# Performance work log

Measured on AMD Instinct MI355X. Metric: run time of the kernel, lower is better.

Reference implementation:

```python
import jax, jax.numpy as jnp
import numpy as np

N_EMBD = 1024
N_HEAD = 16

def _lin_params(key, fan_in, fan_out):
    kw, kb = jax.random.split(key)
    bound = 1.0 / np.sqrt(fan_in)
    W = jax.random.uniform(kw, (fan_in, fan_out), minval=-bound, maxval=bound, dtype=jnp.float32)
    b = jax.random.uniform(kb, (fan_out,), minval=-bound, maxval=bound, dtype=jnp.float32)
    return W, b

def setup_inputs() -> dict:
    key = jax.random.key(0)
    ks = jax.random.split(key, 6)
    x = jax.random.normal(ks[0], (2, 2048, N_EMBD), dtype=jnp.float32)
    W_attn, b_attn = _lin_params(ks[1], N_EMBD, 3 * N_EMBD)
    W_proj, b_proj = _lin_params(ks[2], N_EMBD, N_EMBD)
    W_fc, b_fc = _lin_params(ks[3], N_EMBD, 4 * N_EMBD)
    W_fc2, b_fc2 = _lin_params(ks[4], 4 * N_EMBD, N_EMBD)
    ln1_g = jnp.ones((N_EMBD,), jnp.float32); ln1_b = jnp.zeros((N_EMBD,), jnp.float32)
    ln2_g = jnp.ones((N_EMBD,), jnp.float32); ln2_b = jnp.zeros((N_EMBD,), jnp.float32)
    return {"x": x, "W_attn": W_attn, "b_attn": b_attn, "W_proj": W_proj, "b_proj": b_proj,
            "W_fc": W_fc, "b_fc": b_fc, "W_fc2": W_fc2, "b_fc2": b_fc2,
            "ln1_g": ln1_g, "ln1_b": ln1_b, "ln2_g": ln2_g, "ln2_b": ln2_b}

def _layernorm(x, g, b, eps=1e-5):
    mu = jnp.mean(x, axis=-1, keepdims=True)
    var = jnp.var(x, axis=-1, keepdims=True)
    return (x - mu) * jax.lax.rsqrt(var + eps) * g + b

def _attention(x, W_attn, b_attn, W_proj, b_proj):
    B, T, C = x.shape
    hd = C // N_HEAD
    qkv = x @ W_attn + b_attn                      # [B,T,3C]
    q, k, v = jnp.split(qkv, 3, axis=-1)
    # [B,T,C] -> [B,H,T,hd]
    q = q.reshape(B, T, N_HEAD, hd).transpose(0, 2, 1, 3)
    k = k.reshape(B, T, N_HEAD, hd).transpose(0, 2, 1, 3)
    v = v.reshape(B, T, N_HEAD, hd).transpose(0, 2, 1, 3)
    att = jnp.einsum('bhqd,bhkd->bhqk', q, k) * (1.0 / np.sqrt(hd))
    causal = jnp.tril(jnp.ones((T, T), bool))
    att = jnp.where(causal[None, None], att, -jnp.inf)
    att = jax.nn.softmax(att, axis=-1)
    y = jnp.einsum('bhqk,bhkd->bhqd', att, v)      # [B,H,T,hd]
    y = y.transpose(0, 2, 1, 3).reshape(B, T, C)
    return y @ W_proj + b_proj

def _mlp(x, W_fc, b_fc, W_fc2, b_fc2):
    h = jax.nn.gelu(x @ W_fc + b_fc, approximate=False)
    return h @ W_fc2 + b_fc2

def reference(x, W_attn, b_attn, W_proj, b_proj, W_fc, b_fc, W_fc2, b_fc2,
              ln1_g, ln1_b, ln2_g, ln2_b):
    x = x + _attention(_layernorm(x, ln1_g, ln1_b), W_attn, b_attn, W_proj, b_proj)
    x = x + _mlp(_layernorm(x, ln2_g, ln2_b), W_fc, b_fc, W_fc2, b_fc2)
    return x
```

## Files before the change

kernel.cpp:

```cpp
#include <hip/hip_runtime.h>
#include <cstdint>
#include <cstddef>


typedef unsigned short u16;
typedef short bf16x8 __attribute__((ext_vector_type(8)));
typedef float f32x4 __attribute__((ext_vector_type(4)));

#define C_EMBD 1024
#define T_SEQ  2048
#define N_BATCH 2
#define N_HEADS 16
#define HEAD_D 64
#define M_TOK  4096
#define Q_SCALE 0.18033688011112042f

__device__ __forceinline__ u16 f2b(float f) {
  union { float f; unsigned u; } v; v.f = f;
  unsigned r = (v.u + 0x7fffu + ((v.u >> 16) & 1u)) >> 16;
  return (u16)r;
}
__device__ __forceinline__ float b2f(u16 u) {
  union { unsigned u; float f; } v; v.u = ((unsigned)u) << 16;
  return v.f;
}
__device__ __forceinline__ unsigned pk2(float a, float b) {
  union { float f; unsigned u; } x, y; x.f = a; y.f = b;
  return __builtin_amdgcn_perm(y.u, x.u, 0x07060302u);
}
__device__ __forceinline__ void load_lds16(const void* g, void* l) {
  __builtin_amdgcn_global_load_lds(
      (const __attribute__((address_space(1))) void*)g,
      (__attribute__((address_space(3))) void*)l, 16, 0, 0);
}
__device__ __forceinline__ float gelu_fast(float x) {
  const float p = x * __builtin_fmaf(0.044715f * x, x, 1.0f);
  const float t = __builtin_amdgcn_exp2f(2.3021859215f * p);
  return x * t * __builtin_amdgcn_rcpf(t + 1.0f);
}

__global__ __launch_bounds__(256) void transpose_cast_all(
    const float* __restrict__ W0, u16* __restrict__ D0,
    const float* __restrict__ W1, u16* __restrict__ D1,
    const float* __restrict__ W2, u16* __restrict__ D2,
    const float* __restrict__ W3, u16* __restrict__ D3) {
  int id = blockIdx.x;
  const float* W; u16* D; int K, N, t;
  if (id < 3072)      { W = W0; D = D0; K = 1024; N = 3072; t = id; }
  else if (id < 4096) { W = W1; D = D1; K = 1024; N = 1024; t = id - 3072; }
  else if (id < 8192) { W = W2; D = D2; K = 1024; N = 4096; t = id - 4096; }
  else                { W = W3; D = D3; K = 4096; N = 1024; t = id - 8192; }
  const int nTN = N >> 5;
  const int n0 = (t % nTN) * 32, k0 = (t / nTN) * 32;
  __shared__ float tile[32][33];
  const int tx = threadIdx.x & 31, ty = threadIdx.x >> 5;
#pragma unroll
  for (int i = 0; i < 32; i += 8)
    tile[ty + i][tx] = W[(size_t)(k0 + ty + i) * N + n0 + tx];
  __syncthreads();
#pragma unroll
  for (int i = 0; i < 32; i += 8)
    D[(size_t)(n0 + ty + i) * K + k0 + tx] = f2b(tile[tx][ty + i]);
}

__global__ __launch_bounds__(256) void ln_cast(
    const float* __restrict__ X, const float* __restrict__ g,
    const float* __restrict__ b, u16* __restrict__ Y) {
  const int row = blockIdx.x;
  const int tid = threadIdx.x;
  const float4 v = ((const float4*)(X + (size_t)row * C_EMBD))[tid];
  float s = v.x + v.y + v.z + v.w;
  float ss = v.x * v.x + v.y * v.y + v.z * v.z + v.w * v.w;
#pragma unroll
  for (int off = 32; off > 0; off >>= 1) {
    s += __shfl_down(s, off, 64);
    ss += __shfl_down(ss, off, 64);
  }
  __shared__ float red[8];
  __shared__ float stats[2];
  const int wave = tid >> 6, lane = tid & 63;
  if (lane == 0) { red[wave] = s; red[4 + wave] = ss; }
  __syncthreads();
  if (tid == 0) {
    float S = red[0] + red[1] + red[2] + red[3];
    float SS = red[4] + red[5] + red[6] + red[7];
    float mu = S * (1.0f / C_EMBD);
    float var = SS * (1.0f / C_EMBD) - mu * mu;
    stats[0] = mu;
    stats[1] = rsqrtf(var + 1e-5f);
  }
  __syncthreads();
  const float mu = stats[0], rs = stats[1];
  const float4 gv = ((const float4*)g)[tid];
  const float4 bv = ((const float4*)b)[tid];
  ushort4 o;
  o.x = f2b((v.x - mu) * rs * gv.x + bv.x);
  o.y = f2b((v.y - mu) * rs * gv.y + bv.y);
  o.z = f2b((v.z - mu) * rs * gv.z + bv.z);
  o.w = f2b((v.w - mu) * rs * gv.w + bv.w);
  ((ushort4*)(Y + (size_t)row * C_EMBD))[tid] = o;
}

__global__ __launch_bounds__(256) void ln_reduce_cast(
    const float* __restrict__ P0, const float* __restrict__ P1,
    const float* __restrict__ bias, const float* __restrict__ res,
    const float* __restrict__ g, const float* __restrict__ b,
    float* __restrict__ X1, u16* __restrict__ Y) {
  const int row = blockIdx.x;
  const int tid = threadIdx.x;
  const size_t base = (size_t)row * C_EMBD;
  const float4 p0 = ((const float4*)(P0 + base))[tid];
  const float4 p1 = ((const float4*)(P1 + base))[tid];
  const float4 rr = ((const float4*)(res + base))[tid];
  const float4 bb = ((const float4*)bias)[tid];
  float4 v;
  v.x = p0.x + p1.x + rr.x + bb.x;
  v.y = p0.y + p1.y + rr.y + bb.y;
  v.z = p0.z + p1.z + rr.z + bb.z;
  v.w = p0.w + p1.w + rr.w + bb.w;
  ((float4*)(X1 + base))[tid] = v;
  float s = v.x + v.y + v.z + v.w;
  float ss = v.x * v.x + v.y * v.y + v.z * v.z + v.w * v.w;
#pragma unroll
  for (int off = 32; off > 0; off >>= 1) {
    s += __shfl_down(s, off, 64);
    ss += __shfl_down(ss, off, 64);
  }
  __shared__ float red[8];
  __shared__ float stats[2];
  const int wave = tid >> 6, lane = tid & 63;
  if (lane == 0) { red[wave] = s; red[4 + wave] = ss; }
  __syncthreads();
  if (tid == 0) {
    float S = red[0] + red[1] + red[2] + red[3];
    float SS = red[4] + red[5] + red[6] + red[7];
    float mu = S * (1.0f / C_EMBD);
    float var = SS * (1.0f / C_EMBD) - mu * mu;
    stats[0] = mu;
    stats[1] = rsqrtf(var + 1e-5f);
  }
  __syncthreads();
  const float mu = stats[0], rs = stats[1];
  const float4 gv = ((const float4*)g)[tid];
  const float4 bv = ((const float4*)b)[tid];
  ushort4 o;
  o.x = f2b((v.x - mu) * rs * gv.x + bv.x);
  o.y = f2b((v.y - mu) * rs * gv.y + bv.y);
  o.z = f2b((v.z - mu) * rs * gv.z + bv.z);
  o.w = f2b((v.w - mu) * rs * gv.w + bv.w);
  ((ushort4*)(Y + base))[tid] = o;
}

enum { EPI_BF16 = 0, EPI_GELU_BF16 = 2, EPI_PART = 3, EPI_QKV = 4 };

template <int EPI, int SPLIT>
__global__ __launch_bounds__(256) void gemm_bt(
    const u16* __restrict__ A, const u16* __restrict__ Bt,
    const float* __restrict__ bias,
    void* __restrict__ Cout, void* __restrict__ Cout2, void* __restrict__ Cout3,
    int M, int N, int K) {
  __shared__ u16 As[128 * 64];
  __shared__ u16 Bs[128 * 64];
  const int tid = threadIdx.x;
  const int wave = tid >> 6, lane = tid & 63;
  const int quad = lane >> 4, l16 = lane & 15;
  const int sw = l16 & 7;

  const int id = (int)blockIdx.y * (int)gridDim.x + (int)blockIdx.x;
  const int mt = ((id & 7) << 2) + ((id >> 3) & 3);
  const int nt_ = id >> 5;
  const int m0 = mt * 128, n0 = nt_ * 128;

  const int wm = (wave >> 1) * 64, wn = (wave & 1) * 64;

  f32x4 acc[4][4] = {};

  size_t aOff[4], bOff[4];
  int ldsOff[4];
#pragma unroll
  for (int i = 0; i < 4; ++i) {
    const int c = tid + i * 256;
    const int row = c >> 3, gc = ((c & 7) ^ (row & 7)) * 8;
    aOff[i] = (size_t)(m0 + row) * K + gc;
    bOff[i] = (size_t)(n0 + row) * K + gc;
    ldsOff[i] = c * 8;
  }

  const int kTiles = (K >> 6) / SPLIT;
  const int kt0 = (SPLIT == 2) ? (int)blockIdx.z * kTiles : 0;
  for (int kt = kt0; kt < kt0 + kTiles; ++kt) {
    const int k0 = kt << 6;
#pragma unroll
    for (int i = 0; i < 4; ++i)
      load_lds16(A + aOff[i] + k0, &As[ldsOff[i]]);
#pragma unroll
    for (int i = 0; i < 4; ++i)
      load_lds16(Bt + bOff[i] + k0, &Bs[ldsOff[i]]);
    __syncthreads();
#pragma unroll
    for (int ks = 0; ks < 2; ++ks) {
      bf16x8 aF[4], bF[4];
#pragma unroll
      for (int t = 0; t < 4; ++t) {
        aF[t] = *(const bf16x8*)
            &As[(wm + t * 16 + l16) * 64 + (((ks * 4 + quad) ^ sw) * 8)];
        bF[t] = *(const bf16x8*)
            &Bs[(wn + t * 16 + l16) * 64 + (((ks * 4 + quad) ^ sw) * 8)];
      }
#pragma unroll
      for (int tm = 0; tm < 4; ++tm)
#pragma unroll
        for (int tn = 0; tn < 4; ++tn)
          acc[tm][tn] = __builtin_amdgcn_mfma_f32_16x16x32_bf16(
              bF[tn], aF[tm], acc[tm][tn], 0, 0, 0);
    }
    __syncthreads();
  }

  float* Pz = (float*)((SPLIT == 2 && blockIdx.z == 1) ? Cout2 : Cout);
#pragma unroll
  for (int tm = 0; tm < 4; ++tm) {
    const int row = m0 + wm + tm * 16 + l16;
#pragma unroll
    for (int tn = 0; tn < 4; ++tn) {
      const int col = n0 + wn + tn * 16 + quad * 4;
      if constexpr (EPI == EPI_PART) {
        *(float4*)&Pz[(size_t)row * N + col] = *(float4*)&acc[tm][tn];
      } else if constexpr (EPI == EPI_QKV) {
        const int bb = row >> 11, t = row & (T_SEQ - 1);
        const float4 bz = *(const float4*)&bias[col];
        float v0 = acc[tm][tn][0] + bz.x, v1 = acc[tm][tn][1] + bz.y;
        float v2 = acc[tm][tn][2] + bz.z, v3 = acc[tm][tn][3] + bz.w;
        const int sec = col >> 10;
        const int h = (col & 1023) >> 6, d4 = col & 63;
        const int bh = bb * N_HEADS + h;
        if (sec == 0) {
          ushort4 o;
          o.x = f2b(v0 * Q_SCALE); o.y = f2b(v1 * Q_SCALE);
          o.z = f2b(v2 * Q_SCALE); o.w = f2b(v3 * Q_SCALE);
          *(ushort4*)&((u16*)Cout)[((size_t)bh * T_SEQ + t) * HEAD_D + d4] = o;
        } else if (sec == 1) {
          ushort4 o;
          o.x = f2b(v0); o.y = f2b(v1); o.z = f2b(v2); o.w = f2b(v3);
          *(ushort4*)&((u16*)Cout2)[((size_t)bh * T_SEQ + t) * HEAD_D + d4] = o;
        } else {
          u16* vp = (u16*)Cout3 + ((size_t)bh * HEAD_D + d4) * T_SEQ + t;
          vp[0] = f2b(v0); vp[T_SEQ] = f2b(v1);
          vp[2 * T_SEQ] = f2b(v2); vp[3 * T_SEQ] = f2b(v3);
        }
      } else {
        const float4 bz = *(const float4*)&bias[col];
        float v0 = acc[tm][tn][0] + bz.x, v1 = acc[tm][tn][1] + bz.y;
        float v2 = acc[tm][tn][2] + bz.z, v3 = acc[tm][tn][3] + bz.w;
        if constexpr (EPI == EPI_GELU_BF16) {
          v0 = gelu_fast(v0); v1 = gelu_fast(v1);
          v2 = gelu_fast(v2); v3 = gelu_fast(v3);
        }
        ushort4 o;
        o.x = f2b(v0); o.y = f2b(v1); o.z = f2b(v2); o.w = f2b(v3);
        *(ushort4*)&((u16*)Cout)[(size_t)row * N + col] = o;
      }
    }
  }
}

__global__ __launch_bounds__(256) void reduce_add(
    const float* __restrict__ P0, const float* __restrict__ P1,
    const float* __restrict__ bias, const float* __restrict__ res,
    float* __restrict__ out) {
  const int idx = blockIdx.x * 256 + threadIdx.x;
  const float4 a = ((const float4*)P0)[idx];
  const float4 b = ((const float4*)P1)[idx];
  const float4 c = ((const float4*)res)[idx];
  const float4 g = ((const float4*)bias)[idx & 255];
  float4 o;
  o.x = a.x + b.x + c.x + g.x;
  o.y = a.y + b.y + c.y + g.y;
  o.z = a.z + b.z + c.z + g.z;
  o.w = a.w + b.w + c.w + g.w;
  ((float4*)out)[idx] = o;
}

__global__ __launch_bounds__(256) void attn_fwd(
    const u16* __restrict__ Q, const u16* __restrict__ Kb,
    const u16* __restrict__ Vt, u16* __restrict__ Y) {
  const int id = (int)blockIdx.y * (int)gridDim.x + (int)blockIdx.x;
  const int bh = (id & 7) + (((id >> 3) & 3) << 3);
  const int pair = id >> 5;
  const int nqt = (int)(T_SEQ / 64);
  const int tid = threadIdx.x;
  const int wave = tid >> 6, lane = tid & 63;
  const int quad = lane >> 4, l16 = lane & 15;
  const int sw = l16 & 7;
  const u16* Qp = Q + (size_t)bh * T_SEQ * HEAD_D;
  const u16* Kp = Kb + (size_t)bh * T_SEQ * HEAD_D;
  const u16* Vp = Vt + (size_t)bh * HEAD_D * T_SEQ;

  __shared__ u16 Ks[2][64 * 64];
  __shared__ u16 Vs[2][64 * 64];
  __shared__ u16 Pl[4][16 * 72];

  const int c1 = tid, c2 = tid + 256;
  const int r1 = c1 >> 3, g1 = ((c1 & 7) ^ (r1 & 7)) * 8;
  const int r2 = c2 >> 3, g2 = ((c2 & 7) ^ (r2 & 7)) * 8;
  const size_t kO1 = (size_t)r1 * HEAD_D + g1, kO2 = (size_t)r2 * HEAD_D + g2;
  const size_t vO1 = (size_t)r1 * T_SEQ + g1, vO2 = (size_t)r2 * T_SEQ + g2;
  u16* const dK1[2] = {&Ks[0][c1 * 8], &Ks[1][c1 * 8]};
  u16* const dK2[2] = {&Ks[0][c2 * 8], &Ks[1][c2 * 8]};
  u16* const dV1[2] = {&Vs[0][c1 * 8], &Vs[1][c1 * 8]};
  u16* const dV2[2] = {&Vs[0][c2 * 8], &Vs[1][c2 * 8]};

  auto stageK = [&](int bb, int k0) {
    const u16* base = Kp + (size_t)k0 * HEAD_D;
    load_lds16(base + kO1, dK1[bb]);
    load_lds16(base + kO2, dK2[bb]);
  };
  auto stageV = [&](int bb, int k0) {
    const u16* base = Vp + k0;
    load_lds16(base + vO1, dV1[bb]);
    load_lds16(base + vO2, dV2[bb]);
  };

  const int b = bh >> 4, h = bh & 15;

#pragma unroll 1
  for (int phase = 0; phase < 2; ++phase) {
    const int qb = phase == 0 ? (nqt - 1 - pair) : pair;
    const int q0 = qb * 64;
    const int qglob = q0 + wave * 16 + l16;

    if (phase == 1) __syncthreads();

    bf16x8 qF[2];
    qF[0] = *(const bf16x8*)&Qp[(size_t)qglob * HEAD_D + quad * 8];
    qF[1] = *(const bf16x8*)&Qp[(size_t)qglob * HEAD_D + 32 + quad * 8];

    f32x4 o[4] = {};
    float mrun = -3e38f, lrun = 0.0f;

    stageK(0, 0);
    stageV(0, 0);

    int buf = 0;
    for (int kb = 0; kb <= qb; ++kb) {
      const int k0 = kb * 64;
      __syncthreads();
      if (kb < qb) {
        stageK(buf ^ 1, k0 + 64);
        stageV(buf ^ 1, k0 + 64);
      }
      f32x4 st[4] = {};
#pragma unroll
      for (int ks = 0; ks < 2; ++ks) {
#pragma unroll
        for (int nt = 0; nt < 4; ++nt) {
          bf16x8 kF = *(const bf16x8*)
              &Ks[buf][(nt * 16 + l16) * 64 + (((ks * 4 + quad) ^ sw) * 8)];
          st[nt] = __builtin_amdgcn_mfma_f32_16x16x32_bf16(kF, qF[ks], st[nt],
                                                           0, 0, 0);
        }
      }
      if (kb == qb) {
#pragma unroll
        for (int nt = 0; nt < 4; ++nt) {
#pragma unroll
          for (int r = 0; r < 4; ++r) {
            const int key = k0 + nt * 16 + quad * 4 + r;
            if (key > qglob) st[nt][r] = -3e38f;
          }
        }
      }
      float m = st[0][0];
#pragma unroll
      for (int nt = 0; nt < 4; ++nt)
#pragma unroll
        for (int r = 0; r < 4; ++r) m = fmaxf(m, st[nt][r]);
      m = fmaxf(m, __shfl_xor(m, 16, 64));
      m = fmaxf(m, __shfl_xor(m, 32, 64));
      const float nm = fmaxf(mrun, m);
      const float alpha = __builtin_amdgcn_exp2f(mrun - nm);
      mrun = nm;
      float sum = 0.0f;
#pragma unroll
      for (int nt = 0; nt < 4; ++nt)
#pragma unroll
        for (int r = 0; r < 4; ++r) {
          const float p = __builtin_amdgcn_exp2f(st[nt][r] - nm);
          st[nt][r] = p;
          sum += p;
        }
      sum += __shfl_xor(sum, 16, 64);
      sum += __shfl_xor(sum, 32, 64);
      lrun = lrun * alpha + sum;
#pragma unroll
      for (int nt = 0; nt < 4; ++nt)
#pragma unroll
        for (int r = 0; r < 4; ++r) o[nt][r] *= alpha;
#pragma unroll
      for (int nt = 0; nt < 4; ++nt) {
        uint2 pk;
        pk.x = pk2(st[nt][0], st[nt][1]);
        pk.y = pk2(st[nt][2], st[nt][3]);
        *(uint2*)&Pl[wave][l16 * 72 + nt * 16 + quad * 4] = pk;
      }
#pragma unroll
      for (int ks = 0; ks < 2; ++ks) {
        bf16x8 aP = *(const bf16x8*)&Pl[wave][l16 * 72 + ks * 32 + quad * 8];
#pragma unroll
        for (int nt = 0; nt < 4; ++nt) {
          bf16x8 vF = *(const bf16x8*)
              &Vs[buf][(nt * 16 + l16) * 64 + (((ks * 4 + quad) ^ sw) * 8)];
          o[nt] =
              __builtin_amdgcn_mfma_f32_16x16x32_bf16(vF, aP, o[nt], 0, 0, 0);
        }
      }
      buf ^= 1;
    }

    const float rl = 1.0f / lrun;
    u16* yp = Y + ((size_t)(b * T_SEQ + qglob)) * C_EMBD + h * HEAD_D;
#pragma unroll
    for (int nt = 0; nt < 4; ++nt) {
      ushort4 ov;
      ov.x = f2b(o[nt][0] * rl); ov.y = f2b(o[nt][1] * rl);
      ov.z = f2b(o[nt][2] * rl); ov.w = f2b(o[nt][3] * rl);
      *(ushort4*)&yp[nt * 16 + quad * 4] = ov;
    }
  }
}

extern "C" void kernel_launch(void* const* d_in, const int* in_sizes, int n_in,
                              void* d_out, int out_size, void* d_ws,
                              size_t ws_size, hipStream_t stream) {
  const float* x      = (const float*)d_in[0];
  const float* W_attn = (const float*)d_in[1];
  const float* b_attn = (const float*)d_in[2];
  const float* W_proj = (const float*)d_in[3];
  const float* b_proj = (const float*)d_in[4];
  const float* W_fc   = (const float*)d_in[5];
  const float* b_fc   = (const float*)d_in[6];
  const float* W_fc2  = (const float*)d_in[7];
  const float* b_fc2  = (const float*)d_in[8];
  const float* ln1_g  = (const float*)d_in[9];
  const float* ln1_b  = (const float*)d_in[10];
  const float* ln2_g  = (const float*)d_in[11];
  const float* ln2_b  = (const float*)d_in[12];

  u16* wqkvT = (u16*)d_ws;
  u16* wprojT = wqkvT + (size_t)3072 * 1024;
  u16* wfcT  = wprojT + (size_t)1024 * 1024;
  u16* wfc2T = wfcT + (size_t)4096 * 1024;
  u16* Abuf  = wfc2T + (size_t)1024 * 4096;
  float* x1  = (float*)(Abuf + (size_t)M_TOK * C_EMBD);
  u16* hbuf  = (u16*)(x1 + (size_t)M_TOK * C_EMBD);
  float* projP = (float*)hbuf;
  u16* Qb    = hbuf + (size_t)M_TOK * 4096;
  u16* Kbuf  = Qb + (size_t)32 * T_SEQ * HEAD_D;
  u16* Vtb   = Kbuf + (size_t)32 * T_SEQ * HEAD_D;
  float* fc2P1 = (float*)Qb;

  const dim3 blk(256);

  transpose_cast_all<<<12288, blk, 0, stream>>>(
      W_attn, wqkvT, W_proj, wprojT, W_fc, wfcT, W_fc2, wfc2T);

  ln_cast<<<M_TOK, blk, 0, stream>>>(x, ln1_g, ln1_b, Abuf);

  gemm_bt<EPI_QKV, 1><<<dim3(3072 / 128, M_TOK / 128), blk, 0, stream>>>(
      Abuf, wqkvT, b_attn, Qb, Kbuf, Vtb, M_TOK, 3072, 1024);

  attn_fwd<<<dim3(T_SEQ / 128, 32), blk, 0, stream>>>(Qb, Kbuf, Vtb, Abuf);

  gemm_bt<EPI_PART, 2><<<dim3(1024 / 128, M_TOK / 128, 2), blk, 0, stream>>>(
      Abuf, wprojT, nullptr, projP, projP + (size_t)M_TOK * C_EMBD, nullptr,
      M_TOK, 1024, 1024);
  ln_reduce_cast<<<M_TOK, blk, 0, stream>>>(
      projP, projP + (size_t)M_TOK * C_EMBD, b_proj, x, ln2_g, ln2_b,
      x1, Abuf);

  gemm_bt<EPI_GELU_BF16, 1><<<dim3(4096 / 128, M_TOK / 128), blk, 0, stream>>>(
      Abuf, wfcT, b_fc, hbuf, nullptr, nullptr, M_TOK, 4096, 1024);

  gemm_bt<EPI_PART, 2><<<dim3(1024 / 128, M_TOK / 128, 2), blk, 0, stream>>>(
      hbuf, wfc2T, nullptr, d_out, fc2P1, nullptr, M_TOK, 1024, 4096);
  reduce_add<<<M_TOK * C_EMBD / 1024, blk, 0, stream>>>(
      (const float*)d_out, fc2P1, b_fc2, x1, (float*)d_out);
}
```

Baseline: 341.7 us.

## Add 256x256 ping-pong GEMM kernel for QKV, FC and FC2 with split-K 4

```diff
diff --git a/kernel.cpp b/kernel.cpp
--- a/kernel.cpp
+++ b/kernel.cpp
@@ -226,28 +226,6 @@
       const int col = n0 + wn + tn * 16 + quad * 4;
       if constexpr (EPI == EPI_PART) {
         *(float4*)&Pz[(size_t)row * N + col] = *(float4*)&acc[tm][tn];
-      } else if constexpr (EPI == EPI_QKV) {
-        const int bb = row >> 11, t = row & (T_SEQ - 1);
-        const float4 bz = *(const float4*)&bias[col];
-        float v0 = acc[tm][tn][0] + bz.x, v1 = acc[tm][tn][1] + bz.y;
-        float v2 = acc[tm][tn][2] + bz.z, v3 = acc[tm][tn][3] + bz.w;
-        const int sec = col >> 10;
-        const int h = (col & 1023) >> 6, d4 = col & 63;
-        const int bh = bb * N_HEADS + h;
-        if (sec == 0) {
-          ushort4 o;
-          o.x = f2b(v0 * Q_SCALE); o.y = f2b(v1 * Q_SCALE);
-          o.z = f2b(v2 * Q_SCALE); o.w = f2b(v3 * Q_SCALE);
-          *(ushort4*)&((u16*)Cout)[((size_t)bh * T_SEQ + t) * HEAD_D + d4] = o;
-        } else if (sec == 1) {
-          ushort4 o;
-          o.x = f2b(v0); o.y = f2b(v1); o.z = f2b(v2); o.w = f2b(v3);
-          *(ushort4*)&((u16*)Cout2)[((size_t)bh * T_SEQ + t) * HEAD_D + d4] = o;
-        } else {
-          u16* vp = (u16*)Cout3 + ((size_t)bh * HEAD_D + d4) * T_SEQ + t;
-          vp[0] = f2b(v0); vp[T_SEQ] = f2b(v1);
-          vp[2 * T_SEQ] = f2b(v2); vp[3 * T_SEQ] = f2b(v3);
-        }
       } else {
         const float4 bz = *(const float4*)&bias[col];
         float v0 = acc[tm][tn][0] + bz.x, v1 = acc[tm][tn][1] + bz.y;
@@ -264,20 +242,203 @@
   }
 }
 
-__global__ __launch_bounds__(256) void reduce_add(
+#define PHASE(MQ, NQ, STG, POST)                                              \
+  {                                                                           \
+    bf16x8 aF[4][2], bF[2][2];                                                \
+    const u16* Ab_ = &lds[(size_t)((((MQ)*2 + par)) << 13)];                  \
+    const u16* Bb_ = &lds[(size_t)(((2 + (NQ)) * 2 + par) << 13)];            \
+    _Pragma("unroll") for (int t_ = 0; t_ < 4; ++t_)                          \
+      _Pragma("unroll") for (int ks = 0; ks < 2; ++ks)                        \
+        aF[t_][ks] = *(const bf16x8*)&Ab_[(wm * 64 + t_ * 16 + l16) * 64 +    \
+                                          (((ks * 4 + quad) ^ sw) << 3)];     \
+    _Pragma("unroll") for (int u_ = 0; u_ < 2; ++u_)                          \
+      _Pragma("unroll") for (int ks = 0; ks < 2; ++ks)                        \
+        bF[u_][ks] = *(const bf16x8*)&Bb_[(wn * 32 + u_ * 16 + l16) * 64 +    \
+                                          (((ks * 4 + quad) ^ sw) << 3)];     \
+    STG;                                                                      \
+    __builtin_amdgcn_s_barrier();                                             \
+    asm volatile("s_waitcnt lgkmcnt(0)" ::: "memory");                        \
+    __builtin_amdgcn_s_setprio(1);                                            \
+    _Pragma("unroll") for (int t_ = 0; t_ < 4; ++t_)                          \
+      _Pragma("unroll") for (int u_ = 0; u_ < 2; ++u_)                        \
+        _Pragma("unroll") for (int ks = 0; ks < 2; ++ks)                      \
+          acc[(MQ)*4 + t_][(NQ)*2 + u_] =                                     \
+              __builtin_amdgcn_mfma_f32_16x16x32_bf16(                        \
+                  bF[u_][ks], aF[t_][ks], acc[(MQ)*4 + t_][(NQ)*2 + u_],      \
+                  0, 0, 0);                                                   \
+    __builtin_amdgcn_s_setprio(0);                                            \
+    POST;                                                                     \
+    __builtin_amdgcn_s_barrier();                                             \
+  }
+
+template <int EPI, int SPLIT>
+__global__ __launch_bounds__(512, 2) void gemm256(
+    const u16* __restrict__ A, const u16* __restrict__ Bt,
+    const float* __restrict__ bias,
+    void* __restrict__ Cout, void* __restrict__ Cout2,
+    void* __restrict__ Cout3, void* __restrict__ Cout4,
+    int M, int N, int K) {
+  __shared__ u16 lds[8 * 8192];
+  const int tid = threadIdx.x;
+  const int lane = tid & 63;
+  const int wave = tid >> 6;
+  const int quad = lane >> 4, l16 = lane & 15;
+  const int sw = l16 & 7;
+  const int wm = wave >> 2, wn = wave & 3;
+
+  const int nwg = (int)gridDim.x;
+  const int rawid = (int)blockIdx.x;
+  const int id = (rawid & 7) * (nwg >> 3) + (rawid >> 3);
+  const int nTM = M >> 8;
+  const int mt = id % nTM, ntl = id / nTM;
+  const int m0 = mt << 8, n0 = ntl << 8;
+
+  f32x4 acc[8][4] = {};
+
+  size_t aOffs[2][2], bOffs[2][2];
+  int ldsc[2];
+#pragma unroll
+  for (int i = 0; i < 2; ++i) {
+    const int c = tid + i * 512;
+    const int r = c >> 3;
+    const int scc = ((c & 7) ^ (r & 7)) << 3;
+    ldsc[i] = c * 8;
+    const int ra = ((r >> 6) << 7) + (r & 63);
+    const int rb = ((r >> 5) << 6) + (r & 31);
+    aOffs[0][i] = (size_t)(m0 + ra) * K + scc;
+    aOffs[1][i] = (size_t)(m0 + ra + 64) * K + scc;
+    bOffs[0][i] = (size_t)(n0 + rb) * K + scc;
+    bOffs[1][i] = (size_t)(n0 + rb + 32) * K + scc;
+  }
+  auto stA = [&](int mq, int p, int kt) {
+    u16* dst = &lds[(size_t)((mq * 2 + p) << 13)];
+    const int k0 = kt << 6;
+#pragma unroll
+    for (int i = 0; i < 2; ++i)
+      load_lds16(A + aOffs[mq][i] + k0, dst + ldsc[i]);
+  };
+  auto stB = [&](int nq, int p, int kt) {
+    u16* dst = &lds[(size_t)(((2 + nq) * 2 + p) << 13)];
+    const int k0 = kt << 6;
+#pragma unroll
+    for (int i = 0; i < 2; ++i)
+      load_lds16(Bt + bOffs[nq][i] + k0, dst + ldsc[i]);
+  };
+
+  const int NT = (K >> 6) / SPLIT;
+  const int kt0 = (SPLIT > 1) ? (int)blockIdx.z * NT : 0;
+
+  stA(0, 0, kt0); stB(0, 0, kt0); stA(1, 0, kt0); stB(1, 0, kt0);
+  stB(0, 1, kt0 + 1); stA(0, 1, kt0 + 1);
+  asm volatile("s_waitcnt vmcnt(4)" ::: "memory");
+  __builtin_amdgcn_s_barrier();
+
+  for (int t = 0; t < NT; t += 2) {
+    {
+      const int par = 0;
+      const int k1 = kt0 + (t + 1 < NT ? t + 1 : 0);
+      const int k2 = kt0 + (t + 2 < NT ? t + 2 : 0);
+      PHASE(0, 0, stA(1, 1, k1), );
+      PHASE(1, 0, stB(1, 1, k1), );
+      PHASE(0, 1, stB(0, 0, k2), );
+      PHASE(1, 1, stA(0, 0, k2),
+            asm volatile("s_waitcnt vmcnt(4)" ::: "memory"));
+    }
+    {
+      const int par = 1;
+      const int k1 = kt0 + (t + 2 < NT ? t + 2 : 0);
+      const int k2 = kt0 + (t + 3 < NT ? t + 3 : 0);
+      PHASE(0, 0, stA(1, 0, k1), );
+      PHASE(1, 0, stB(1, 0, k1), );
+      PHASE(0, 1, stB(0, 1, k2), );
+      PHASE(1, 1, stA(0, 1, k2),
+            asm volatile("s_waitcnt vmcnt(4)" ::: "memory"));
+    }
+  }
+  asm volatile("s_waitcnt vmcnt(0)" ::: "memory");
+
+  if constexpr (EPI == EPI_PART) {
+    const int z = (SPLIT > 1) ? (int)blockIdx.z : 0;
+    float* Pz = (float*)(z == 0 ? Cout : z == 1 ? Cout2
+                                       : z == 2 ? Cout3 : Cout4);
+#pragma unroll
+    for (int tm = 0; tm < 8; ++tm) {
+      const int row = m0 + wm * 128 + tm * 16 + l16;
+#pragma unroll
+      for (int tn = 0; tn < 4; ++tn) {
+        const int col = n0 + wn * 64 + tn * 16 + quad * 4;
+        *(float4*)&Pz[(size_t)row * N + col] = *(float4*)&acc[tm][tn];
+      }
+    }
+  } else if constexpr (EPI == EPI_QKV) {
+#pragma unroll
+    for (int tm = 0; tm < 8; ++tm) {
+      const int row = m0 + wm * 128 + tm * 16 + l16;
+      const int bb = row >> 11, tt = row & (T_SEQ - 1);
+#pragma unroll
+      for (int tn = 0; tn < 4; ++tn) {
+        const int col = n0 + wn * 64 + tn * 16 + quad * 4;
+        const float4 bz = *(const float4*)&bias[col];
+        float v0 = acc[tm][tn][0] + bz.x, v1 = acc[tm][tn][1] + bz.y;
+        float v2 = acc[tm][tn][2] + bz.z, v3 = acc[tm][tn][3] + bz.w;
+        const int sec = col >> 10;
+        const int h = (col & 1023) >> 6, d4 = col & 63;
+        const int bh = bb * N_HEADS + h;
+        if (sec == 0) {
+          ushort4 o;
+          o.x = f2b(v0 * Q_SCALE); o.y = f2b(v1 * Q_SCALE);
+          o.z = f2b(v2 * Q_SCALE); o.w = f2b(v3 * Q_SCALE);
+          *(ushort4*)&((u16*)Cout)[((size_t)bh * T_SEQ + tt) * HEAD_D + d4] = o;
+        } else if (sec == 1) {
+          ushort4 o;
+          o.x = f2b(v0); o.y = f2b(v1); o.z = f2b(v2); o.w = f2b(v3);
+          *(ushort4*)&((u16*)Cout2)[((size_t)bh * T_SEQ + tt) * HEAD_D + d4] = o;
+        } else {
+          u16* vp = (u16*)Cout3 + ((size_t)bh * HEAD_D + d4) * T_SEQ + tt;
+          vp[0] = f2b(v0); vp[T_SEQ] = f2b(v1);
+          vp[2 * T_SEQ] = f2b(v2); vp[3 * T_SEQ] = f2b(v3);
+        }
+      }
+    }
+  } else {
+#pragma unroll
+    for (int tm = 0; tm < 8; ++tm) {
+      const int row = m0 + wm * 128 + tm * 16 + l16;
+#pragma unroll
+      for (int tn = 0; tn < 4; ++tn) {
+        const int col = n0 + wn * 64 + tn * 16 + quad * 4;
+        const float4 bz = *(const float4*)&bias[col];
+        float v0 = acc[tm][tn][0] + bz.x, v1 = acc[tm][tn][1] + bz.y;
+        float v2 = acc[tm][tn][2] + bz.z, v3 = acc[tm][tn][3] + bz.w;
+        if constexpr (EPI == EPI_GELU_BF16) {
+          v0 = gelu_fast(v0); v1 = gelu_fast(v1);
+          v2 = gelu_fast(v2); v3 = gelu_fast(v3);
+        }
+        ushort4 o;
+        o.x = f2b(v0); o.y = f2b(v1); o.z = f2b(v2); o.w = f2b(v3);
+        *(ushort4*)&((u16*)Cout)[(size_t)row * N + col] = o;
+      }
+    }
+  }
+}
+
+__global__ __launch_bounds__(256) void reduce_add4(
     const float* __restrict__ P0, const float* __restrict__ P1,
+    const float* __restrict__ P2, const float* __restrict__ P3,
     const float* __restrict__ bias, const float* __restrict__ res,
     float* __restrict__ out) {
   const int idx = blockIdx.x * 256 + threadIdx.x;
   const float4 a = ((const float4*)P0)[idx];
   const float4 b = ((const float4*)P1)[idx];
-  const float4 c = ((const float4*)res)[idx];
+  const float4 c = ((const float4*)P2)[idx];
+  const float4 d = ((const float4*)P3)[idx];
+  const float4 r = ((const float4*)res)[idx];
   const float4 g = ((const float4*)bias)[idx & 255];
   float4 o;
-  o.x = a.x + b.x + c.x + g.x;
-  o.y = a.y + b.y + c.y + g.y;
-  o.z = a.z + b.z + c.z + g.z;
-  o.w = a.w + b.w + c.w + g.w;
+  o.x = a.x + b.x + c.x + d.x + r.x + g.x;
+  o.y = a.y + b.y + c.y + d.y + r.y + g.y;
+  o.z = a.z + b.z + c.z + d.z + r.z + g.z;
+  o.w = a.w + b.w + c.w + d.w + r.w + g.w;
   ((float4*)out)[idx] = o;
 }
 
@@ -446,28 +607,33 @@
   const float* ln2_g  = (const float*)d_in[11];
   const float* ln2_b  = (const float*)d_in[12];
 
-  u16* wqkvT = (u16*)d_ws;
+  u16* wfc2T = (u16*)d_ws;
+  float* x1  = (float*)(wfc2T + (size_t)1024 * 4096);
+  u16* hbuf  = (u16*)(x1 + (size_t)M_TOK * C_EMBD);
+  u16* dead  = hbuf + (size_t)M_TOK * 4096;
+  u16* wqkvT = dead;
   u16* wprojT = wqkvT + (size_t)3072 * 1024;
   u16* wfcT  = wprojT + (size_t)1024 * 1024;
-  u16* wfc2T = wfcT + (size_t)4096 * 1024;
-  u16* Abuf  = wfc2T + (size_t)1024 * 4096;
-  float* x1  = (float*)(Abuf + (size_t)M_TOK * C_EMBD);
-  u16* hbuf  = (u16*)(x1 + (size_t)M_TOK * C_EMBD);
-  float* projP = (float*)hbuf;
-  u16* Qb    = hbuf + (size_t)M_TOK * 4096;
+  u16* Abuf  = wfcT + (size_t)4096 * 1024;
+  u16* Qb    = Abuf + (size_t)M_TOK * C_EMBD;
   u16* Kbuf  = Qb + (size_t)32 * T_SEQ * HEAD_D;
   u16* Vtb   = Kbuf + (size_t)32 * T_SEQ * HEAD_D;
-  float* fc2P1 = (float*)Qb;
+
+  float* projP = (float*)hbuf;
+  float* fc2P1 = (float*)dead;
+  float* fc2P2 = fc2P1 + (size_t)M_TOK * C_EMBD;
+  float* fc2P3 = fc2P2 + (size_t)M_TOK * C_EMBD;
 
   const dim3 blk(256);
+  const dim3 blk512(512);
 
   transpose_cast_all<<<12288, blk, 0, stream>>>(
       W_attn, wqkvT, W_proj, wprojT, W_fc, wfcT, W_fc2, wfc2T);
 
   ln_cast<<<M_TOK, blk, 0, stream>>>(x, ln1_g, ln1_b, Abuf);
 
-  gemm_bt<EPI_QKV, 1><<<dim3(3072 / 128, M_TOK / 128), blk, 0, stream>>>(
-      Abuf, wqkvT, b_attn, Qb, Kbuf, Vtb, M_TOK, 3072, 1024);
+  gemm256<EPI_QKV, 1><<<dim3(192), blk512, 0, stream>>>(
+      Abuf, wqkvT, b_attn, Qb, Kbuf, Vtb, nullptr, M_TOK, 3072, 1024);
 
   attn_fwd<<<dim3(T_SEQ / 128, 32), blk, 0, stream>>>(Qb, Kbuf, Vtb, Abuf);
 
@@ -478,11 +644,11 @@
       projP, projP + (size_t)M_TOK * C_EMBD, b_proj, x, ln2_g, ln2_b,
       x1, Abuf);
 
-  gemm_bt<EPI_GELU_BF16, 1><<<dim3(4096 / 128, M_TOK / 128), blk, 0, stream>>>(
-      Abuf, wfcT, b_fc, hbuf, nullptr, nullptr, M_TOK, 4096, 1024);
-
-  gemm_bt<EPI_PART, 2><<<dim3(1024 / 128, M_TOK / 128, 2), blk, 0, stream>>>(
-      hbuf, wfc2T, nullptr, d_out, fc2P1, nullptr, M_TOK, 1024, 4096);
-  reduce_add<<<M_TOK * C_EMBD / 1024, blk, 0, stream>>>(
-      (const float*)d_out, fc2P1, b_fc2, x1, (float*)d_out);
-}
+  gemm256<EPI_GELU_BF16, 1><<<dim3(256), blk512, 0, stream>>>(
+      Abuf, wfcT, b_fc, hbuf, nullptr, nullptr, nullptr, M_TOK, 4096, 1024);
+
+  gemm256<EPI_PART, 4><<<dim3(64, 1, 4), blk512, 0, stream>>>(
+      hbuf, wfc2T, nullptr, d_out, fc2P1, fc2P2, fc2P3, M_TOK, 1024, 4096);
+  reduce_add4<<<M_TOK * C_EMBD / 1024, blk, 0, stream>>>(
+      (const float*)d_out, fc2P1, fc2P2, fc2P3, b_fc2, x1, (float*)d_out);
+}
```

After: 343.5 us. About the same (+0.5%).
